# Performance work log

Measured on AMD Instinct MI355X. Metric: run time of the kernel, lower is better.

## Reference

```python
import jax, jax.numpy as jnp
import numpy as np

N = 50000          # num_nodes
F_IN = 128         # node_features
H = 256            # hidden_dim
H_OUT = H // 2     # 128
E = 800000         # num_edges (avg degree 16)
LN_EPS = 1e-5


def _glorot(key, fan_in, fan_out):
    lim = np.sqrt(6.0 / (fan_in + fan_out))
    return jax.random.uniform(key, (fan_in, fan_out), jnp.float32, -lim, lim)


def setup_inputs() -> dict:
    key = jax.random.key(0)
    ks = jax.random.split(key, 8)
    node_ids = jnp.arange(N, dtype=jnp.int64 if jax.config.jax_enable_x64 else jnp.int32)
    edge_index = jax.random.randint(ks[0], (2, E), 0, N, dtype=jnp.int32)
    emb = jax.random.normal(ks[1], (N, F_IN), jnp.float32)
    W1 = _glorot(ks[2], F_IN, H)
    b1 = jnp.zeros((H,), jnp.float32)
    W2 = _glorot(ks[3], H, H)
    b2 = jnp.zeros((H,), jnp.float32)
    W3 = _glorot(ks[4], H, H_OUT)
    b3 = jnp.zeros((H_OUT,), jnp.float32)
    gamma = jnp.ones((H_OUT,), jnp.float32)
    beta = jnp.zeros((H_OUT,), jnp.float32)
    return {"node_ids": node_ids, "edge_index": edge_index, "emb": emb,
            "W1": W1, "b1": b1, "W2": W2, "b2": b2, "W3": W3, "b3": b3,
            "gamma": gamma, "beta": beta}


def _gcn_norm(edge_index):
    # PyG GCNConv default: add self-loops, symmetric normalization D^-1/2 A D^-1/2
    loop = jnp.arange(N, dtype=edge_index.dtype)
    src = jnp.concatenate([edge_index[0], loop])  # [E + N]
    dst = jnp.concatenate([edge_index[1], loop])
    deg = jax.ops.segment_sum(jnp.ones_like(dst, jnp.float32), dst, num_segments=N)
    dinv = jnp.where(deg > 0, jax.lax.rsqrt(deg), 0.0)
    norm = dinv[src] * dinv[dst]  # [E + N]
    return src, dst, norm


def _gcn_conv(x, src, dst, norm, W, b):
    h = x @ W                               # [N, d_out] transform first (PyG order)
    msg = h[src] * norm[:, None]            # gather + scale  [E+N, d_out]
    out = jax.ops.segment_sum(msg, dst, num_segments=N)  # scatter-add
    return out + b


def _layer_norm(x, gamma, beta):
    mu = jnp.mean(x, axis=-1, keepdims=True)
    var = jnp.mean(jnp.square(x - mu), axis=-1, keepdims=True)
    return (x - mu) * jax.lax.rsqrt(var + LN_EPS) * gamma + beta


def reference(node_ids, edge_index, emb, W1, b1, W2, b2, W3, b3, gamma, beta):
    src, dst, norm = _gcn_norm(edge_index)
    x = emb[node_ids]                       # embedding lookup [N, F_IN]
    x = jax.nn.relu(_gcn_conv(x, src, dst, norm, W1, b1))
    # dropout is identity in eval mode
    x = jax.nn.relu(_gcn_conv(x, src, dst, norm, W2, b2))
    x = _gcn_conv(x, src, dst, norm, W3, b3)
    return _layer_norm(x, gamma, beta)
```

## Files before the change

### kernel.cpp

```cpp
#include <hip/hip_runtime.h>
#include <hip/hip_bf16.h>


#define N_NODES 50000
#define BLK 256

__global__ void k_indeg(const int* __restrict__ dst, int* __restrict__ indeg, int E) {
    int e = blockIdx.x * blockDim.x + threadIdx.x;
    if (e < E) atomicAdd(&indeg[dst[e]], 1);
}

#define SCAN_T 1024
__global__ void k_scan(const int* __restrict__ indeg, int* __restrict__ rowptr, int n) {
    __shared__ int sh[SCAN_T];
    __shared__ int s_carry;
    int tid = threadIdx.x;
    if (tid == 0) s_carry = 0;
    __syncthreads();
    const int CHUNK = SCAN_T * 8;
    for (int base = 0; base < n; base += CHUNK) {
        int loc[8]; int lsum = 0;
#pragma unroll
        for (int j = 0; j < 8; ++j) {
            int idx = base + tid * 8 + j;
            loc[j] = (idx < n) ? indeg[idx] : 0;
            lsum += loc[j];
        }
        sh[tid] = lsum;
        __syncthreads();
        for (int off = 1; off < SCAN_T; off <<= 1) {
            int t = (tid >= off) ? sh[tid - off] : 0;
            __syncthreads();
            sh[tid] += t;
            __syncthreads();
        }
        int excl = s_carry + sh[tid] - lsum;
        int total = s_carry + sh[SCAN_T - 1];
#pragma unroll
        for (int j = 0; j < 8; ++j) {
            int idx = base + tid * 8 + j;
            if (idx < n) rowptr[idx] = excl;
            excl += loc[j];
        }
        __syncthreads();
        if (tid == 0) s_carry = total;
        __syncthreads();
    }
    if (tid == 0) rowptr[n] = s_carry;
}

__global__ void k_fill(const int* __restrict__ src, const int* __restrict__ dst,
                       const int* __restrict__ rowptr, int* __restrict__ cursor,
                       int* __restrict__ col, int E) {
    int e = blockIdx.x * blockDim.x + threadIdx.x;
    if (e < E) {
        int d = dst[e];
        int pos = rowptr[d] + atomicAdd(&cursor[d], 1);
        col[pos] = src[e];
    }
}

__global__ void k_dinv(const int* __restrict__ indeg, float* __restrict__ dinv, int n) {
    int i = blockIdx.x * blockDim.x + threadIdx.x;
    if (i < n) dinv[i] = rsqrtf((float)indeg[i] + 1.0f);
}

__global__ void k_prescale(const float* __restrict__ emb, const int* __restrict__ ids,
                           const float* __restrict__ dinv, float* __restrict__ xs, int n) {
    int t = blockIdx.x * blockDim.x + threadIdx.x;
    if (t >= n * 32) return;
    int node = t >> 5, lane = t & 31;
    int s = ids[node];
    float4 v = ((const float4*)emb)[(size_t)s * 32 + lane];
    float di = dinv[node];
    ((float4*)xs)[(size_t)node * 32 + lane] = make_float4(v.x*di, v.y*di, v.z*di, v.w*di);
}

template<int D, int EPI>
__global__ __launch_bounds__(BLK) void k_agg(const float* __restrict__ H,
        const int* __restrict__ rowptr, const int* __restrict__ col,
        const float* __restrict__ dinv, const float* __restrict__ bias,
        float* __restrict__ out, int n) {
    constexpr int LPN = D / 4;
    int t = blockIdx.x * blockDim.x + threadIdx.x;
    int node = t / LPN;
    int lane = t % LPN;
    if (node >= n) return;
    const float4* Hv = (const float4*)H;
    float4 acc = Hv[(size_t)node * LPN + lane];
    int beg = rowptr[node], end = rowptr[node + 1];
    for (int e = beg; e < end; ++e) {
        int s = col[e];
        float4 v = Hv[(size_t)s * LPN + lane];
        acc.x += v.x; acc.y += v.y; acc.z += v.z; acc.w += v.w;
    }
    float di = dinv[node];
    float4 r;
    if constexpr (EPI == 0) {
        r = make_float4(acc.x*di, acc.y*di, acc.z*di, acc.w*di);
    } else {
        float4 b = ((const float4*)bias)[lane];
        r.x = fmaxf(fmaf(acc.x, di, b.x), 0.f);
        r.y = fmaxf(fmaf(acc.y, di, b.y), 0.f);
        r.z = fmaxf(fmaf(acc.z, di, b.z), 0.f);
        r.w = fmaxf(fmaf(acc.w, di, b.w), 0.f);
    }
    ((float4*)out)[(size_t)node * LPN + lane] = r;
}

__global__ __launch_bounds__(BLK) void k_agg_ln(const float* __restrict__ H,
        const int* __restrict__ rowptr, const int* __restrict__ col,
        const float* __restrict__ dinv, const float* __restrict__ b3,
        const float* __restrict__ gamma, const float* __restrict__ beta,
        float* __restrict__ out, int n) {
    int gt = blockIdx.x * blockDim.x + threadIdx.x;
    int node = gt >> 6;
    int lane = gt & 63;
    if (node >= n) return;
    const float2* Hv = (const float2*)H;
    float2 acc = Hv[(size_t)node * 64 + lane];
    int beg = rowptr[node], end = rowptr[node + 1];
    for (int e = beg; e < end; ++e) {
        int s = col[e];
        float2 v = Hv[(size_t)s * 64 + lane];
        acc.x += v.x; acc.y += v.y;
    }
    float di = dinv[node];
    int f0 = lane * 2;
    float t0 = fmaf(acc.x, di, b3[f0]);
    float t1 = fmaf(acc.y, di, b3[f0 + 1]);
    float s = t0 + t1, sq = t0*t0 + t1*t1;
#pragma unroll
    for (int off = 32; off >= 1; off >>= 1) {
        s  += __shfl_xor(s, off, 64);
        sq += __shfl_xor(sq, off, 64);
    }
    float mu  = s * (1.0f / 128.0f);
    float var = sq * (1.0f / 128.0f) - mu * mu;
    float inv = rsqrtf(var + 1e-5f);
    float2 o;
    o.x = fmaf((t0 - mu) * inv, gamma[f0],     beta[f0]);
    o.y = fmaf((t1 - mu) * inv, gamma[f0 + 1], beta[f0 + 1]);
    ((float2*)out)[(size_t)node * 64 + lane] = o;
}

template<int EPI>
__global__ __launch_bounds__(256) void k_gemm(const float* __restrict__ A,
        const float* __restrict__ B, const float* __restrict__ bias,
        const float* __restrict__ dinv, float* __restrict__ C,
        int M, int N, int K) {
    constexpr int BM = 128, BN = 128, BK = 16;
    __shared__ float As[BK][BM];
    __shared__ float Bs[BK][BN];
    int m0 = blockIdx.x * BM;
    int n0 = blockIdx.y * BN;
    int tid = threadIdx.x;
    int tx = tid & 15, ty = tid >> 4;
    int ar  = tid >> 2;
    int akq = tid & 3;
    int bk  = tid >> 5;
    int bnc = tid & 31;
    float acc[8][8] = {};
    for (int k0 = 0; k0 < K; k0 += BK) {
#pragma unroll
        for (int h = 0; h < 2; ++h) {
            int row = ar + h * 64;
            int gm = m0 + row;
            float4 v = make_float4(0.f, 0.f, 0.f, 0.f);
            if (gm < M) v = *(const float4*)&A[(size_t)gm * K + k0 + akq * 4];
            As[akq*4+0][row] = v.x;
            As[akq*4+1][row] = v.y;
            As[akq*4+2][row] = v.z;
            As[akq*4+3][row] = v.w;
        }
#pragma unroll
        for (int h = 0; h < 2; ++h) {
            int kr = bk + h * 8;
            float4 v = *(const float4*)&B[(size_t)(k0 + kr) * N + n0 + bnc * 4];
            *(float4*)&Bs[kr][bnc * 4] = v;
        }
        __syncthreads();
#pragma unroll
        for (int kk = 0; kk < BK; ++kk) {
            float a[8], b[8];
            *(float4*)&a[0] = *(const float4*)&As[kk][ty * 4];
            *(float4*)&a[4] = *(const float4*)&As[kk][64 + ty * 4];
            *(float4*)&b[0] = *(const float4*)&Bs[kk][tx * 4];
            *(float4*)&b[4] = *(const float4*)&Bs[kk][64 + tx * 4];
#pragma unroll
            for (int i = 0; i < 8; ++i)
#pragma unroll
                for (int j = 0; j < 8; ++j)
                    acc[i][j] = fmaf(a[i], b[j], acc[i][j]);
        }
        __syncthreads();
    }
#pragma unroll
    for (int i = 0; i < 8; ++i) {
        int row = m0 + ((i < 4) ? (ty * 4 + i) : (64 + ty * 4 + i - 4));
        if (row >= M) continue;
        float sc = (EPI == 1) ? dinv[row] : 0.f;
#pragma unroll
        for (int h = 0; h < 2; ++h) {
            int c0 = n0 + h * 64 + tx * 4;
            const float* ac = &acc[i][h * 4];
            float4 o;
            if constexpr (EPI == 0) {
                o.x = fmaxf(ac[0] + bias[c0+0], 0.f);
                o.y = fmaxf(ac[1] + bias[c0+1], 0.f);
                o.z = fmaxf(ac[2] + bias[c0+2], 0.f);
                o.w = fmaxf(ac[3] + bias[c0+3], 0.f);
            } else {
                o = make_float4(ac[0]*sc, ac[1]*sc, ac[2]*sc, ac[3]*sc);
            }
            *(float4*)&C[(size_t)row * N + c0] = o;
        }
    }
}

static inline size_t align256(size_t x) { return (x + 255) & ~(size_t)255; }

extern "C" void kernel_launch(void* const* d_in, const int* in_sizes, int n_in,
                              void* d_out, int out_size, void* d_ws, size_t ws_size,
                              hipStream_t stream) {
    const int*   node_ids = (const int*)  d_in[0];
    const int*   ei       = (const int*)  d_in[1];
    const float* emb      = (const float*)d_in[2];
    const float* W1       = (const float*)d_in[3];
    const float* b1       = (const float*)d_in[4];
    const float* W2       = (const float*)d_in[5];
    const float* b2       = (const float*)d_in[6];
    const float* W3       = (const float*)d_in[7];
    const float* b3       = (const float*)d_in[8];
    const float* gamma    = (const float*)d_in[9];
    const float* beta     = (const float*)d_in[10];
    float* out = (float*)d_out;

    const int N = in_sizes[0];
    const int E = in_sizes[1] / 2;
    const int* esrc = ei;
    const int* edst = ei + E;

    char* p = (char*)d_ws;
    size_t off = 0;
    int*   indeg  = (int*)(p + off);  off = align256(off + (size_t)N * 4);
    int*   rowptr = (int*)(p + off);  off = align256(off + (size_t)(N + 1) * 4);
    int*   cursor = (int*)(p + off);  off = align256(off + (size_t)N * 4);
    float* dinv   = (float*)(p + off); off = align256(off + (size_t)N * 4);
    int*   col    = (int*)(p + off);  off = align256(off + (size_t)E * 4);
    float* bufC   = (float*)(p + off); off = align256(off + (size_t)N * 128 * 4);
    float* bufA   = (float*)(p + off); off = align256(off + (size_t)N * 256 * 4);
    float* bufB   = (float*)(p + off); off = align256(off + (size_t)N * 256 * 4);

    hipMemsetAsync(indeg, 0, (size_t)N * 4, stream);
    hipMemsetAsync(cursor, 0, (size_t)N * 4, stream);

    int eb = (E + BLK - 1) / BLK;
    k_indeg<<<eb, BLK, 0, stream>>>(edst, indeg, E);
    k_scan<<<1, SCAN_T, 0, stream>>>(indeg, rowptr, N);
    k_fill<<<eb, BLK, 0, stream>>>(esrc, edst, rowptr, cursor, col, E);
    k_dinv<<<(N + BLK - 1) / BLK, BLK, 0, stream>>>(indeg, dinv, N);

    k_prescale<<<(N * 32 + BLK - 1) / BLK, BLK, 0, stream>>>(emb, node_ids, dinv, bufC, N);
    k_agg<128, 0><<<(N * 32 + BLK - 1) / BLK, BLK, 0, stream>>>(bufC, rowptr, col, dinv, nullptr, bufA, N);
    {
        dim3 g((N + 127) / 128, 256 / 128);
        k_gemm<0><<<g, 256, 0, stream>>>(bufA, W1, b1, nullptr, bufB, N, 256, 128);
    }
    {
        dim3 g((N + 127) / 128, 256 / 128);
        k_gemm<1><<<g, 256, 0, stream>>>(bufB, W2, nullptr, dinv, bufA, N, 256, 256);
    }
    k_agg<256, 1><<<(N * 64 + BLK - 1) / BLK, BLK, 0, stream>>>(bufA, rowptr, col, dinv, b2, bufB, N);
    {
        dim3 g((N + 127) / 128, 128 / 128);
        k_gemm<1><<<g, 256, 0, stream>>>(bufB, W3, nullptr, dinv, bufC, N, 128, 256);
    }
    k_agg_ln<<<(N * 64 + BLK - 1) / BLK, BLK, 0, stream>>>(bufC, rowptr, col, dinv, b3, gamma, beta, out, N);
}
```

Before: 722.5 us.

## Use split-bf16 MFMA GEMMs, unroll gather loops, and warp-shuffle scan

Measured after the change: 586.2 us. -18.9%, faster.

```diff
diff --git a/kernel.cpp b/kernel.cpp
--- a/kernel.cpp
+++ b/kernel.cpp
@@ -2,8 +2,23 @@
 #include <hip/hip_bf16.h>
 
 
-#define N_NODES 50000
 #define BLK 256
+
+typedef __attribute__((ext_vector_type(8))) short bf16x8;
+typedef __attribute__((ext_vector_type(4))) float f32x4;
+typedef unsigned short u16;
+typedef unsigned int u32;
+
+__device__ inline u16 f2b_rne(float v) {
+    u32 x = __float_as_uint(v);
+    u32 r = (x + 0x7FFFu + ((x >> 16) & 1u)) >> 16;
+    return (u16)r;
+}
+__device__ inline void split_bf(float v, u16& h, u16& l) {
+    h = f2b_rne(v);
+    float fh = __uint_as_float((u32)h << 16);
+    l = f2b_rne(v - fh);
+}
 
 __global__ void k_indeg(const int* __restrict__ dst, int* __restrict__ indeg, int E) {
     int e = blockIdx.x * blockDim.x + threadIdx.x;
@@ -12,39 +27,49 @@
 
 #define SCAN_T 1024
 __global__ void k_scan(const int* __restrict__ indeg, int* __restrict__ rowptr, int n) {
-    __shared__ int sh[SCAN_T];
+    __shared__ int s_wsum[16];
+    __shared__ int s_wpre[16];
     __shared__ int s_carry;
-    int tid = threadIdx.x;
+    int tid = threadIdx.x, lane = tid & 63, wid = tid >> 6;
     if (tid == 0) s_carry = 0;
     __syncthreads();
     const int CHUNK = SCAN_T * 8;
     for (int base = 0; base < n; base += CHUNK) {
+        int idx0 = base + tid * 8;
         int loc[8]; int lsum = 0;
 #pragma unroll
         for (int j = 0; j < 8; ++j) {
-            int idx = base + tid * 8 + j;
+            int idx = idx0 + j;
             loc[j] = (idx < n) ? indeg[idx] : 0;
             lsum += loc[j];
         }
-        sh[tid] = lsum;
-        __syncthreads();
-        for (int off = 1; off < SCAN_T; off <<= 1) {
-            int t = (tid >= off) ? sh[tid - off] : 0;
-            __syncthreads();
-            sh[tid] += t;
-            __syncthreads();
-        }
-        int excl = s_carry + sh[tid] - lsum;
-        int total = s_carry + sh[SCAN_T - 1];
+        int sc = lsum;
+#pragma unroll
+        for (int off = 1; off < 64; off <<= 1) {
+            int t = __shfl_up(sc, off, 64);
+            if (lane >= off) sc += t;
+        }
+        if (lane == 63) s_wsum[wid] = sc;
+        __syncthreads();
+        if (tid < 16) {
+            int w = s_wsum[tid];
+#pragma unroll
+            for (int off = 1; off < 16; off <<= 1) {
+                int t = __shfl_up(w, off, 64);
+                if (tid >= off) w += t;
+            }
+            s_wpre[tid] = w;
+        }
+        __syncthreads();
+        int excl = s_carry + (wid ? s_wpre[wid - 1] : 0) + sc - lsum;
 #pragma unroll
         for (int j = 0; j < 8; ++j) {
-            int idx = base + tid * 8 + j;
+            int idx = idx0 + j;
             if (idx < n) rowptr[idx] = excl;
             excl += loc[j];
         }
         __syncthreads();
-        if (tid == 0) s_carry = total;
-        __syncthreads();
+        if (tid == 0) s_carry += s_wpre[15];
     }
     if (tid == 0) rowptr[n] = s_carry;
 }
@@ -63,6 +88,16 @@
 __global__ void k_dinv(const int* __restrict__ indeg, float* __restrict__ dinv, int n) {
     int i = blockIdx.x * blockDim.x + threadIdx.x;
     if (i < n) dinv[i] = rsqrtf((float)indeg[i] + 1.0f);
+}
+
+__global__ void k_wprep(const float* __restrict__ W, u16* __restrict__ Whi,
+                        u16* __restrict__ Wlo, int K, int N) {
+    int idx = blockIdx.x * blockDim.x + threadIdx.x;
+    if (idx >= K * N) return;
+    int nn = idx / K, kk = idx - nn * K;
+    float v = W[(size_t)kk * N + nn];
+    u16 h, l; split_bf(v, h, l);
+    Whi[idx] = h; Wlo[idx] = l;
 }
 
 __global__ void k_prescale(const float* __restrict__ emb, const int* __restrict__ ids,
@@ -76,11 +111,11 @@
     ((float4*)xs)[(size_t)node * 32 + lane] = make_float4(v.x*di, v.y*di, v.z*di, v.w*di);
 }
 
-template<int D, int EPI>
+template<int D, int EPI, int OUT>
 __global__ __launch_bounds__(BLK) void k_agg(const float* __restrict__ H,
         const int* __restrict__ rowptr, const int* __restrict__ col,
         const float* __restrict__ dinv, const float* __restrict__ bias,
-        float* __restrict__ out, int n) {
+        float* __restrict__ outf, u16* __restrict__ outh, u16* __restrict__ outl, int n) {
     constexpr int LPN = D / 4;
     int t = blockIdx.x * blockDim.x + threadIdx.x;
     int node = t / LPN;
@@ -88,8 +123,19 @@
     if (node >= n) return;
     const float4* Hv = (const float4*)H;
     float4 acc = Hv[(size_t)node * LPN + lane];
-    int beg = rowptr[node], end = rowptr[node + 1];
-    for (int e = beg; e < end; ++e) {
+    int e = rowptr[node], end = rowptr[node + 1];
+    for (; e + 4 <= end; e += 4) {
+        int s0 = col[e], s1 = col[e+1], s2 = col[e+2], s3 = col[e+3];
+        float4 v0 = Hv[(size_t)s0 * LPN + lane];
+        float4 v1 = Hv[(size_t)s1 * LPN + lane];
+        float4 v2 = Hv[(size_t)s2 * LPN + lane];
+        float4 v3 = Hv[(size_t)s3 * LPN + lane];
+        acc.x += (v0.x + v1.x) + (v2.x + v3.x);
+        acc.y += (v0.y + v1.y) + (v2.y + v3.y);
+        acc.z += (v0.z + v1.z) + (v2.z + v3.z);
+        acc.w += (v0.w + v1.w) + (v2.w + v3.w);
+    }
+    for (; e < end; ++e) {
         int s = col[e];
         float4 v = Hv[(size_t)s * LPN + lane];
         acc.x += v.x; acc.y += v.y; acc.z += v.z; acc.w += v.w;
@@ -105,7 +151,17 @@
         r.z = fmaxf(fmaf(acc.z, di, b.z), 0.f);
         r.w = fmaxf(fmaf(acc.w, di, b.w), 0.f);
     }
-    ((float4*)out)[(size_t)node * LPN + lane] = r;
+    if constexpr (OUT == 0) {
+        ((float4*)outf)[(size_t)node * LPN + lane] = r;
+    } else {
+        ushort4 h4, l4;
+        split_bf(r.x, h4.x, l4.x);
+        split_bf(r.y, h4.y, l4.y);
+        split_bf(r.z, h4.z, l4.z);
+        split_bf(r.w, h4.w, l4.w);
+        ((ushort4*)outh)[(size_t)node * LPN + lane] = h4;
+        ((ushort4*)outl)[(size_t)node * LPN + lane] = l4;
+    }
 }
 
 __global__ __launch_bounds__(BLK) void k_agg_ln(const float* __restrict__ H,
@@ -119,8 +175,17 @@
     if (node >= n) return;
     const float2* Hv = (const float2*)H;
     float2 acc = Hv[(size_t)node * 64 + lane];
-    int beg = rowptr[node], end = rowptr[node + 1];
-    for (int e = beg; e < end; ++e) {
+    int e = rowptr[node], end = rowptr[node + 1];
+    for (; e + 4 <= end; e += 4) {
+        int s0 = col[e], s1 = col[e+1], s2 = col[e+2], s3 = col[e+3];
+        float2 v0 = Hv[(size_t)s0 * 64 + lane];
+        float2 v1 = Hv[(size_t)s1 * 64 + lane];
+        float2 v2 = Hv[(size_t)s2 * 64 + lane];
+        float2 v3 = Hv[(size_t)s3 * 64 + lane];
+        acc.x += (v0.x + v1.x) + (v2.x + v3.x);
+        acc.y += (v0.y + v1.y) + (v2.y + v3.y);
+    }
+    for (; e < end; ++e) {
         int s = col[e];
         float2 v = Hv[(size_t)s * 64 + lane];
         acc.x += v.x; acc.y += v.y;
@@ -145,75 +210,86 @@
 }
 
 template<int EPI>
-__global__ __launch_bounds__(256) void k_gemm(const float* __restrict__ A,
-        const float* __restrict__ B, const float* __restrict__ bias,
-        const float* __restrict__ dinv, float* __restrict__ C,
+__global__ __launch_bounds__(256) void k_gemm_bf3(
+        const u16* __restrict__ Ahi, const u16* __restrict__ Alo,
+        const u16* __restrict__ Bhi, const u16* __restrict__ Blo,
+        const float* __restrict__ bias, const float* __restrict__ dinv,
+        float* __restrict__ Cf, u16* __restrict__ Chi, u16* __restrict__ Clo,
         int M, int N, int K) {
-    constexpr int BM = 128, BN = 128, BK = 16;
-    __shared__ float As[BK][BM];
-    __shared__ float Bs[BK][BN];
-    int m0 = blockIdx.x * BM;
-    int n0 = blockIdx.y * BN;
+    __shared__ u16 sA[2][128 * 64];
+    __shared__ u16 sB[2][128 * 64];
+    int m0 = blockIdx.x * 128;
+    int n0 = blockIdx.y * 128;
     int tid = threadIdx.x;
-    int tx = tid & 15, ty = tid >> 4;
-    int ar  = tid >> 2;
-    int akq = tid & 3;
-    int bk  = tid >> 5;
-    int bnc = tid & 31;
-    float acc[8][8] = {};
-    for (int k0 = 0; k0 < K; k0 += BK) {
-#pragma unroll
-        for (int h = 0; h < 2; ++h) {
-            int row = ar + h * 64;
+    int lane = tid & 63, wid = tid >> 6;
+    int wm = wid >> 1, wn = wid & 1;
+    int r16 = lane & 15, kg = lane >> 4;
+    f32x4 acc[4][4] = {};
+    for (int k0 = 0; k0 < K; k0 += 64) {
+        for (int c = tid; c < 1024; c += 256) {
+            int row = c >> 3, slot = c & 7;
+            int sl = slot ^ (row & 7);
             int gm = m0 + row;
-            float4 v = make_float4(0.f, 0.f, 0.f, 0.f);
-            if (gm < M) v = *(const float4*)&A[(size_t)gm * K + k0 + akq * 4];
-            As[akq*4+0][row] = v.x;
-            As[akq*4+1][row] = v.y;
-            As[akq*4+2][row] = v.z;
-            As[akq*4+3][row] = v.w;
-        }
-#pragma unroll
-        for (int h = 0; h < 2; ++h) {
-            int kr = bk + h * 8;
-            float4 v = *(const float4*)&B[(size_t)(k0 + kr) * N + n0 + bnc * 4];
-            *(float4*)&Bs[kr][bnc * 4] = v;
-        }
-        __syncthreads();
-#pragma unroll
-        for (int kk = 0; kk < BK; ++kk) {
-            float a[8], b[8];
-            *(float4*)&a[0] = *(const float4*)&As[kk][ty * 4];
-            *(float4*)&a[4] = *(const float4*)&As[kk][64 + ty * 4];
-            *(float4*)&b[0] = *(const float4*)&Bs[kk][tx * 4];
-            *(float4*)&b[4] = *(const float4*)&Bs[kk][64 + tx * 4];
-#pragma unroll
-            for (int i = 0; i < 8; ++i)
-#pragma unroll
-                for (int j = 0; j < 8; ++j)
-                    acc[i][j] = fmaf(a[i], b[j], acc[i][j]);
-        }
-        __syncthreads();
-    }
-#pragma unroll
-    for (int i = 0; i < 8; ++i) {
-        int row = m0 + ((i < 4) ? (ty * 4 + i) : (64 + ty * 4 + i - 4));
-        if (row >= M) continue;
-        float sc = (EPI == 1) ? dinv[row] : 0.f;
-#pragma unroll
-        for (int h = 0; h < 2; ++h) {
-            int c0 = n0 + h * 64 + tx * 4;
-            const float* ac = &acc[i][h * 4];
-            float4 o;
-            if constexpr (EPI == 0) {
-                o.x = fmaxf(ac[0] + bias[c0+0], 0.f);
-                o.y = fmaxf(ac[1] + bias[c0+1], 0.f);
-                o.z = fmaxf(ac[2] + bias[c0+2], 0.f);
-                o.w = fmaxf(ac[3] + bias[c0+3], 0.f);
-            } else {
-                o = make_float4(ac[0]*sc, ac[1]*sc, ac[2]*sc, ac[3]*sc);
-            }
-            *(float4*)&C[(size_t)row * N + c0] = o;
+            uint4 vh = make_uint4(0u,0u,0u,0u), vl = vh;
+            if (gm < M) {
+                size_t g = (size_t)gm * K + k0 + slot * 8;
+                vh = *(const uint4*)(Ahi + g);
+                vl = *(const uint4*)(Alo + g);
+            }
+            *(uint4*)&sA[0][row * 64 + sl * 8] = vh;
+            *(uint4*)&sA[1][row * 64 + sl * 8] = vl;
+            size_t gb = (size_t)(n0 + row) * K + k0 + slot * 8;
+            *(uint4*)&sB[0][row * 64 + sl * 8] = *(const uint4*)(Bhi + gb);
+            *(uint4*)&sB[1][row * 64 + sl * 8] = *(const uint4*)(Blo + gb);
+        }
+        __syncthreads();
+#pragma unroll
+        for (int kk = 0; kk < 2; ++kk) {
+            bf16x8 ah[4], al[4], bh[4], bl[4];
+#pragma unroll
+            for (int f = 0; f < 4; ++f) {
+                int ar = wm * 64 + f * 16 + r16;
+                int asl = (kk * 4 + kg) ^ (ar & 7);
+                ah[f] = *(const bf16x8*)&sA[0][ar * 64 + asl * 8];
+                al[f] = *(const bf16x8*)&sA[1][ar * 64 + asl * 8];
+                int br = wn * 64 + f * 16 + r16;
+                int bsl = (kk * 4 + kg) ^ (br & 7);
+                bh[f] = *(const bf16x8*)&sB[0][br * 64 + bsl * 8];
+                bl[f] = *(const bf16x8*)&sB[1][br * 64 + bsl * 8];
+            }
+#pragma unroll
+            for (int i = 0; i < 4; ++i)
+#pragma unroll
+            for (int j = 0; j < 4; ++j) {
+                acc[i][j] = __builtin_amdgcn_mfma_f32_16x16x32_bf16(ah[i], bh[j], acc[i][j], 0, 0, 0);
+                acc[i][j] = __builtin_amdgcn_mfma_f32_16x16x32_bf16(ah[i], bl[j], acc[i][j], 0, 0, 0);
+                acc[i][j] = __builtin_amdgcn_mfma_f32_16x16x32_bf16(al[i], bh[j], acc[i][j], 0, 0, 0);
+            }
+        }
+        __syncthreads();
+    }
+#pragma unroll
+    for (int i = 0; i < 4; ++i) {
+#pragma unroll
+        for (int j = 0; j < 4; ++j) {
+            int nn = n0 + wn * 64 + j * 16 + r16;
+            float bv = 0.f;
+            if constexpr (EPI == 0) bv = bias[nn];
+#pragma unroll
+            for (int r = 0; r < 4; ++r) {
+                int mm = m0 + wm * 64 + i * 16 + kg * 4 + r;
+                if (mm >= M) continue;
+                float x = acc[i][j][r];
+                if constexpr (EPI == 0) {
+                    x = fmaxf(x + bv, 0.f);
+                    u16 h, l; split_bf(x, h, l);
+                    size_t o = (size_t)mm * N + nn;
+                    Chi[o] = h; Clo[o] = l;
+                } else {
+                    x *= dinv[mm];
+                    Cf[(size_t)mm * N + nn] = x;
+                }
+            }
         }
     }
 }
@@ -243,14 +319,29 @@
 
     char* p = (char*)d_ws;
     size_t off = 0;
-    int*   indeg  = (int*)(p + off);  off = align256(off + (size_t)N * 4);
-    int*   rowptr = (int*)(p + off);  off = align256(off + (size_t)(N + 1) * 4);
-    int*   cursor = (int*)(p + off);  off = align256(off + (size_t)N * 4);
+    int*   indeg  = (int*)(p + off);   off = align256(off + (size_t)N * 4);
+    int*   rowptr = (int*)(p + off);   off = align256(off + (size_t)(N + 1) * 4);
+    int*   cursor = (int*)(p + off);   off = align256(off + (size_t)N * 4);
     float* dinv   = (float*)(p + off); off = align256(off + (size_t)N * 4);
-    int*   col    = (int*)(p + off);  off = align256(off + (size_t)E * 4);
-    float* bufC   = (float*)(p + off); off = align256(off + (size_t)N * 128 * 4);
-    float* bufA   = (float*)(p + off); off = align256(off + (size_t)N * 256 * 4);
-    float* bufB   = (float*)(p + off); off = align256(off + (size_t)N * 256 * 4);
+    int*   col    = (int*)(p + off);   off = align256(off + (size_t)E * 4);
+    u16* W1thi = (u16*)(p + off); off = align256(off + 256 * 128 * 2);
+    u16* W1tlo = (u16*)(p + off); off = align256(off + 256 * 128 * 2);
+    u16* W2thi = (u16*)(p + off); off = align256(off + 256 * 256 * 2);
+    u16* W2tlo = (u16*)(p + off); off = align256(off + 256 * 256 * 2);
+    u16* W3thi = (u16*)(p + off); off = align256(off + 128 * 256 * 2);
+    u16* W3tlo = (u16*)(p + off); off = align256(off + 128 * 256 * 2);
+    char* S1 = p + off; off = align256(off + (size_t)N * 256 * 4);
+    char* S2 = p + off; off = align256(off + (size_t)N * 256 * 4);
+
+    float* X    = (float*)S1;
+    u16*   H1hi = (u16*)S1;
+    u16*   H1lo = (u16*)(S1 + (size_t)N * 256 * 2);
+    u16*   X2hi = H1hi;
+    u16*   X2lo = H1lo;
+    u16*   A1hi = (u16*)S2;
+    u16*   A1lo = (u16*)(S2 + (size_t)N * 128 * 2);
+    float* G2   = (float*)S2;
+    float* G3   = (float*)S2;
 
     hipMemsetAsync(indeg, 0, (size_t)N * 4, stream);
     hipMemsetAsync(cursor, 0, (size_t)N * 4, stream);
@@ -261,20 +352,23 @@
     k_fill<<<eb, BLK, 0, stream>>>(esrc, edst, rowptr, cursor, col, E);
     k_dinv<<<(N + BLK - 1) / BLK, BLK, 0, stream>>>(indeg, dinv, N);
 
-    k_prescale<<<(N * 32 + BLK - 1) / BLK, BLK, 0, stream>>>(emb, node_ids, dinv, bufC, N);
-    k_agg<128, 0><<<(N * 32 + BLK - 1) / BLK, BLK, 0, stream>>>(bufC, rowptr, col, dinv, nullptr, bufA, N);
-    {
-        dim3 g((N + 127) / 128, 256 / 128);
-        k_gemm<0><<<g, 256, 0, stream>>>(bufA, W1, b1, nullptr, bufB, N, 256, 128);
-    }
-    {
-        dim3 g((N + 127) / 128, 256 / 128);
-        k_gemm<1><<<g, 256, 0, stream>>>(bufB, W2, nullptr, dinv, bufA, N, 256, 256);
-    }
-    k_agg<256, 1><<<(N * 64 + BLK - 1) / BLK, BLK, 0, stream>>>(bufA, rowptr, col, dinv, b2, bufB, N);
-    {
-        dim3 g((N + 127) / 128, 128 / 128);
-        k_gemm<1><<<g, 256, 0, stream>>>(bufB, W3, nullptr, dinv, bufC, N, 128, 256);
-    }
-    k_agg_ln<<<(N * 64 + BLK - 1) / BLK, BLK, 0, stream>>>(bufC, rowptr, col, dinv, b3, gamma, beta, out, N);
-}
+    k_wprep<<<(128 * 256 + 255) / 256, 256, 0, stream>>>(W1, W1thi, W1tlo, 128, 256);
+    k_wprep<<<(256 * 256 + 255) / 256, 256, 0, stream>>>(W2, W2thi, W2tlo, 256, 256);
+    k_wprep<<<(256 * 128 + 255) / 256, 256, 0, stream>>>(W3, W3thi, W3tlo, 256, 128);
+
+    int mg = (N + 127) / 128;
+
+    k_prescale<<<(N * 32 + BLK - 1) / BLK, BLK, 0, stream>>>(emb, node_ids, dinv, X, N);
+    k_agg<128, 0, 1><<<(N * 32 + BLK - 1) / BLK, BLK, 0, stream>>>(
+        X, rowptr, col, dinv, nullptr, nullptr, A1hi, A1lo, N);
+    k_gemm_bf3<0><<<dim3(mg, 2), 256, 0, stream>>>(
+        A1hi, A1lo, W1thi, W1tlo, b1, nullptr, nullptr, H1hi, H1lo, N, 256, 128);
+    k_gemm_bf3<1><<<dim3(mg, 2), 256, 0, stream>>>(
+        H1hi, H1lo, W2thi, W2tlo, nullptr, dinv, G2, nullptr, nullptr, N, 256, 256);
+    k_agg<256, 1, 1><<<(N * 64 + BLK - 1) / BLK, BLK, 0, stream>>>(
+        G2, rowptr, col, dinv, b2, nullptr, X2hi, X2lo, N);
+    k_gemm_bf3<1><<<dim3(mg, 1), 256, 0, stream>>>(
+        X2hi, X2lo, W3thi, W3tlo, nullptr, dinv, G3, nullptr, nullptr, N, 128, 256);
+    k_agg_ln<<<(N * 64 + BLK - 1) / BLK, BLK, 0, stream>>>(
+        G3, rowptr, col, dinv, b3, gamma, beta, out, N);
+}
```
